# Kernel optimization log

Measured on AMD Instinct MI355X. Metric: run time of the kernel, lower is better.

The kernel has to match this reference:

```python
import jax, jax.numpy as jnp
import numpy as np

N, K, C, G = 100000, 16, 64, 8
EPS = 1e-5


def bn(x, gamma, beta):
    # training-mode BatchNorm1d over all dims except channel (last)
    axes = tuple(range(x.ndim - 1))
    m = jnp.mean(x, axis=axes)
    v = jnp.var(x, axis=axes)
    return (x - m) * jax.lax.rsqrt(v + EPS) * gamma + beta


def setup_inputs() -> dict:
    key = jax.random.key(0)
    ks = jax.random.split(key, 16)

    def lin(k, i, o):
        return (jax.random.normal(k, (i, o), jnp.float32) / np.sqrt(i)).astype(jnp.float32)

    feat = jax.random.normal(ks[0], (N, C), jnp.float32)
    coord = jax.random.uniform(ks[1], (N, 3), jnp.float32) * 10.0
    ref = jax.random.randint(ks[2], (N, K), 0, N)
    drop = jax.random.uniform(ks[3], (N, K)) < 0.05  # some padded (-1) neighbors
    ref = jnp.where(drop, -1, ref)

    return {
        "feat": feat, "coord": coord, "reference_index": ref,
        "wq": lin(ks[4], C, C), "bq": jnp.zeros((C,), jnp.float32),
        "gq": jnp.ones((C,), jnp.float32), "betaq": jnp.zeros((C,), jnp.float32),
        "wk": lin(ks[5], C, C), "bk": jnp.zeros((C,), jnp.float32),
        "gk": jnp.ones((C,), jnp.float32), "betak": jnp.zeros((C,), jnp.float32),
        "wv": lin(ks[6], C, C), "bv": jnp.zeros((C,), jnp.float32),
        "wp1": lin(ks[7], 3, C), "bp1": jnp.zeros((C,), jnp.float32),
        "gp": jnp.ones((C,), jnp.float32), "betap": jnp.zeros((C,), jnp.float32),
        "wp2": lin(ks[8], C, C), "bp2": jnp.zeros((C,), jnp.float32),
        "ww1": lin(ks[9], C, G), "bw1": jnp.zeros((G,), jnp.float32),
        "gw": jnp.ones((G,), jnp.float32), "betaw": jnp.zeros((G,), jnp.float32),
        "ww2": lin(ks[10], G, G), "bw2": jnp.zeros((G,), jnp.float32),
    }


def reference(feat, coord, reference_index,
              wq, bq, gq, betaq,
              wk, bk, gk, betak,
              wv, bv,
              wp1, bp1, gp, betap,
              wp2, bp2,
              ww1, bw1, gw, betaw,
              ww2, bw2):
    # q/k/v projections
    q = jax.nn.relu(bn(feat @ wq + bq, gq, betaq))   # [N, C]
    k = jax.nn.relu(bn(feat @ wk + bk, gk, betak))   # [N, C]
    v = feat @ wv + bv                                # [N, C]

    idx = jnp.clip(reference_index, 0, N - 1)         # clipped gather index [N, K]
    mask = (reference_index >= 0).astype(feat.dtype)  # sign(ref + 1)

    key_n = k[idx]                                    # [N, K, C] neighbor keys
    val = v[idx]                                      # [N, K, C]
    pos = coord[idx] - coord[:, None, :]              # [N, K, 3] relative coords

    relation_qk = key_n - q[:, None, :]               # [N, K, C]

    # pe_bias branch
    peb = jax.nn.relu(bn(pos @ wp1 + bp1, gp, betap)) @ wp2 + bp2  # [N, K, C]
    relation_qk = relation_qk + peb
    val = val + peb

    # weight encoding -> grouped softmax over neighbors, masked
    w = jax.nn.relu(bn(relation_qk @ ww1 + bw1, gw, betaw)) @ ww2 + bw2  # [N, K, G]
    w = jax.nn.softmax(w, axis=1) * mask[:, :, None]

    val = val.reshape(N, K, G, C // G)
    out = jnp.einsum('nsgi,nsg->ngi', val, w).reshape(N, C)
    return out
```

## Files before the change

### kernel.cpp

```cpp
#include <hip/hip_runtime.h>
#include <hip/hip_bf16.h>

#define NPTS 100000
#define KNBR 16
#define CCH  64
#define GRP  8
#define BN_EPS 1e-5f
#define NROW (NPTS * KNBR)
#define NBATCH (NROW / 64)
#define NPB   ((NPTS + 63) / 64)

#define O_QLINH 0
#define O_KLINH (NPTS * 32)
#define O_VLINH (NPTS * 64)
#define O_STAT  (NPTS * 96)
#define O_AFF   (O_STAT + 416)
#define O_W2W1  (O_AFF + 416)
#define O_BW1E  (O_W2W1 + 512)
#define O_QW1   (O_BW1E + 8)
#define O_KW1   (O_QW1 + NPTS * 8)
#define O_W1H   (O_KW1 + NPTS * 8)

typedef __attribute__((ext_vector_type(8))) short short8;
typedef __attribute__((ext_vector_type(4))) short short4v;
typedef __attribute__((ext_vector_type(4))) float f32x4;
#define MFMA16(a, b, c) __builtin_amdgcn_mfma_f32_16x16x32_bf16(a, b, c, 0, 0, 0)

__device__ __forceinline__ int clip_idx(int r) {
    int i = r < 0 ? 0 : r;
    return i >= NPTS ? NPTS - 1 : i;
}
__device__ __forceinline__ unsigned short f2bf(float x) {
    union { float f; unsigned u; } v; v.f = x;
    unsigned r = v.u + 0x7fffu + ((v.u >> 16) & 1u);
    return (unsigned short)(r >> 16);
}
__device__ __forceinline__ float bf2f(unsigned short h) {
    union { unsigned u; float f; } v; v.u = ((unsigned)h) << 16;
    return v.f;
}
__device__ __forceinline__ unsigned pk_bf16(float lo, float hi) {
    unsigned r;
    asm("v_cvt_pk_bf16_f32 %0, %1, %2" : "=v"(r) : "v"(lo), "v"(hi));
    return r;
}
__device__ __forceinline__ int physK(int s) {
    return (s >> 5) * 32 + ((s >> 2) & 3) * 8 + ((s >> 4) & 1) * 4 + (s & 3);
}
__device__ __forceinline__ int aOff(int r, int p) {
    return r * 64 + (((p >> 3) ^ (r & 7)) << 3) + (p & 7);
}
__device__ __forceinline__ int kib_of(int i, int q) {
    return (i < 4) ? (4 * q + i) : (16 + 4 * q + (i - 4));
}

__global__ __launch_bounds__(512) void k_prep(
    const float* __restrict__ wp2, const float* __restrict__ ww1,
    const float* __restrict__ bw1, const float* __restrict__ bp2,
    float* __restrict__ stat, float* __restrict__ w2w1, float* __restrict__ bw1e)
{
    int t = threadIdx.x;
    if (t < 416) stat[t] = 0.f;
    int j = t >> 3, g = t & 7;
    float acc = 0.f;
    #pragma unroll 16
    for (int c = 0; c < 64; ++c) acc = fmaf(wp2[j * 64 + c], ww1[c * 8 + g], acc);
    w2w1[t] = acc;
    if (t < 8) {
        float b = bw1[t];
        #pragma unroll 16
        for (int c = 0; c < 64; ++c) b = fmaf(bp2[c], ww1[c * 8 + t], b);
        bw1e[t] = b;
    }
}

#define QKV_BLOCKS 512
__global__ __launch_bounds__(256) void k_qkv(
    const float* __restrict__ feat,
    const float* __restrict__ wq, const float* __restrict__ bq,
    const float* __restrict__ wk, const float* __restrict__ bk,
    const float* __restrict__ wv, const float* __restrict__ bv,
    const float* __restrict__ bp2,
    const float* __restrict__ coord, const int* __restrict__ ref,
    short* __restrict__ QlinH, short* __restrict__ KlinH, short* __restrict__ VlinH,
    float* __restrict__ stat)
{
    __shared__ short sA[4096];
    __shared__ float s_red[9];
    const int tid = threadIdx.x, lane = tid & 63, w = tid >> 6;
    const int q = lane >> 4, c15 = lane & 15;

    if (blockIdx.x >= QKV_BLOCKS) {
        float m[9];
        #pragma unroll
        for (int i = 0; i < 9; ++i) m[i] = 0.f;
        const int gid = (blockIdx.x - QKV_BLOCKS) * 256 + tid;
        const int stride = 128 * 256;
        for (int row = gid; row < NROW; row += stride) {
            int n = row >> 4;
            int idx = clip_idx(ref[row]);
            float px = coord[idx * 3 + 0] - coord[n * 3 + 0];
            float py = coord[idx * 3 + 1] - coord[n * 3 + 1];
            float pz = coord[idx * 3 + 2] - coord[n * 3 + 2];
            m[0] += px; m[1] += py; m[2] += pz;
            m[3] = fmaf(px, px, m[3]); m[4] = fmaf(py, py, m[4]); m[5] = fmaf(pz, pz, m[5]);
            m[6] = fmaf(px, py, m[6]); m[7] = fmaf(px, pz, m[7]); m[8] = fmaf(py, pz, m[8]);
        }
        if (tid < 9) s_red[tid] = 0.f;
        __syncthreads();
        #pragma unroll
        for (int off = 32; off >= 1; off >>= 1) {
            #pragma unroll
            for (int i = 0; i < 9; ++i) m[i] += __shfl_xor(m[i], off, 64);
        }
        if (lane == 0) {
            #pragma unroll
            for (int i = 0; i < 9; ++i) atomicAdd(&s_red[i], m[i]);
        }
        __syncthreads();
        if (tid < 9) atomicAdd(&stat[256 + tid], s_red[tid]);
        return;
    }

    short8 bfrag[3][2];
    float bias[3];
    #pragma unroll
    for (int t = 0; t < 3; ++t) {
        int gt = w * 3 + t;
        const float* W = (gt < 4) ? wq : (gt < 8) ? wk : wv;
        const float* B = (gt < 4) ? bq : (gt < 8) ? bk : bv;
        int col = (gt * 16 + c15) & 63;
        bias[t] = B[col] + (gt >= 8 ? bp2[col] : 0.f);
        #pragma unroll
        for (int kt = 0; kt < 2; ++kt) {
            short8 bb;
            #pragma unroll
            for (int i = 0; i < 8; ++i) {
                int kk = kt * 32 + kib_of(i, q);
                bb[i] = (short)f2bf(W[kk * 64 + col]);
            }
            bfrag[t][kt] = bb;
        }
    }
    float st_s[3], st_q[3];
    #pragma unroll
    for (int t = 0; t < 3; ++t) { st_s[t] = 0.f; st_q[t] = 0.f; }

    const int c4 = c15 * 4;
    const int pk4 = physK(c4);

    for (int b = blockIdx.x; b < NPB; b += QKV_BLOCKS) {
        const int pbase = b * 64;
        #pragma unroll
        for (int i = 0; i < 4; ++i) {
            int p = w * 16 + i * 4 + q;
            int n = pbase + p;
            float4 v = make_float4(0.f, 0.f, 0.f, 0.f);
            if (n < NPTS) v = *(const float4*)(feat + n * 64 + c4);
            short4v h;
            h[0] = (short)f2bf(v.x); h[1] = (short)f2bf(v.y);
            h[2] = (short)f2bf(v.z); h[3] = (short)f2bf(v.w);
            *(short4v*)(sA + aOff(p, pk4)) = h;
        }
        __syncthreads();
        #pragma unroll
        for (int mt = 0; mt < 4; ++mt) {
            int r = mt * 16 + c15;
            int ch0 = q ^ (r & 7);
            int ch1 = (4 + q) ^ (r & 7);
            short8 a0 = *(const short8*)(sA + r * 64 + (ch0 << 3));
            short8 a1 = *(const short8*)(sA + r * 64 + (ch1 << 3));
            #pragma unroll
            for (int t = 0; t < 3; ++t) {
                f32x4 acc = (f32x4){0.f, 0.f, 0.f, 0.f};
                acc = MFMA16(a0, bfrag[t][0], acc);
                acc = MFMA16(a1, bfrag[t][1], acc);
                int gt = w * 3 + t;
                #pragma unroll
                for (int rg = 0; rg < 4; ++rg) {
                    int row = mt * 16 + 4 * q + rg;
                    int n = pbase + row;
                    if (n < NPTS) {
                        unsigned short h = f2bf(acc[rg] + bias[t]);
                        float vr = bf2f(h);
                        if (gt < 4)      QlinH[n * 64 + gt * 16 + c15] = (short)h;
                        else if (gt < 8) KlinH[n * 64 + (gt - 4) * 16 + c15] = (short)h;
                        else             VlinH[n * 64 + (gt - 8) * 16 + c15] = (short)h;
                        if (gt < 8) { st_s[t] += vr; st_q[t] = fmaf(vr, vr, st_q[t]); }
                    }
                }
            }
        }
        __syncthreads();
    }
    #pragma unroll
    for (int t = 0; t < 3; ++t) {
        st_s[t] += __shfl_xor(st_s[t], 16, 64); st_s[t] += __shfl_xor(st_s[t], 32, 64);
        st_q[t] += __shfl_xor(st_q[t], 16, 64); st_q[t] += __shfl_xor(st_q[t], 32, 64);
    }
    if (q == 0) {
        #pragma unroll
        for (int t = 0; t < 3; ++t) {
            int gt = w * 3 + t;
            if (gt < 4) {
                atomicAdd(&stat[gt * 16 + c15], st_s[t]);
                atomicAdd(&stat[64 + gt * 16 + c15], st_q[t]);
            } else if (gt < 8) {
                atomicAdd(&stat[128 + (gt - 4) * 16 + c15], st_s[t]);
                atomicAdd(&stat[192 + (gt - 4) * 16 + c15], st_q[t]);
            }
        }
    }
}

__global__ __launch_bounds__(192) void k_finA(
    const float* __restrict__ gq, const float* __restrict__ betaq,
    const float* __restrict__ gk, const float* __restrict__ betak,
    const float* __restrict__ gp, const float* __restrict__ betap,
    const float* __restrict__ wp1, const float* __restrict__ bp1,
    const float* __restrict__ stat, float* __restrict__ aff)
{
    int t = threadIdx.x;
    if (t < 64) {
        float m = stat[t] / (float)NPTS;
        float v = stat[64 + t] / (float)NPTS - m * m;
        float a = gq[t] * rsqrtf(v + BN_EPS);
        aff[t] = a;
        aff[64 + t] = betaq[t] - m * a;
    } else if (t < 128) {
        int c = t - 64;
        float m = stat[128 + c] / (float)NPTS;
        float v = stat[192 + c] / (float)NPTS - m * m;
        float a = gk[c] * rsqrtf(v + BN_EPS);
        aff[128 + c] = a;
        aff[192 + c] = betak[c] - m * a;
    } else {
        int c = t - 128;
        const float R = (float)NROW;
        float Ex = stat[256] / R, Ey = stat[257] / R, Ez = stat[258] / R;
        float Exx = stat[259] / R, Eyy = stat[260] / R, Ezz = stat[261] / R;
        float Exy = stat[262] / R, Exz = stat[263] / R, Eyz = stat[264] / R;
        float Cxx = Exx - Ex * Ex, Cyy = Eyy - Ey * Ey, Czz = Ezz - Ez * Ez;
        float Cxy = Exy - Ex * Ey, Cxz = Exz - Ex * Ez, Cyz = Eyz - Ey * Ez;
        float a0 = wp1[c], a1 = wp1[64 + c], a2 = wp1[128 + c];
        float mean = a0 * Ex + a1 * Ey + a2 * Ez + bp1[c];
        float var = a0 * a0 * Cxx + a1 * a1 * Cyy + a2 * a2 * Czz
                  + 2.f * (a0 * a1 * Cxy + a0 * a2 * Cxz + a1 * a2 * Cyz);
        float a = gp[c] * rsqrtf(var + BN_EPS);
        aff[256 + c] = a;
        aff[320 + c] = betap[c] - mean * a;
    }
}

__global__ __launch_bounds__(128) void k_qkw(
    const short* __restrict__ QlinH, const short* __restrict__ KlinH,
    const float* __restrict__ ww1, const float* __restrict__ aff,
    float* __restrict__ QW1, float* __restrict__ KW1)
{
    __shared__ short sA[2][8192];
    const int tid = threadIdx.x, lane = tid & 63, w = tid >> 6;
    const int q = lane >> 4, g = lane & 15;
    short8 bimg[2];
    #pragma unroll
    for (int kt = 0; kt < 2; ++kt) {
        short8 bb;
        #pragma unroll
        for (int i = 0; i < 8; ++i) {
            int s = kt * 32 + kib_of(i, q);
            bb[i] = (short)f2bf(g < 8 ? ww1[s * 8 + g] : 0.f);
        }
        bimg[kt] = bb;
    }
    const int r8 = lane >> 3, c8 = (lane & 7) * 8;
    f32x4 qa0 = *(const f32x4*)(aff + c8),       qa1 = *(const f32x4*)(aff + c8 + 4);
    f32x4 qb0 = *(const f32x4*)(aff + 64 + c8),  qb1 = *(const f32x4*)(aff + 64 + c8 + 4);
    f32x4 ka0 = *(const f32x4*)(aff + 128 + c8), ka1 = *(const f32x4*)(aff + 128 + c8 + 4);
    f32x4 kb0 = *(const f32x4*)(aff + 192 + c8), kb1 = *(const f32x4*)(aff + 192 + c8 + 4);
    const int pkA = physK(c8), pkB = physK(c8 + 4);
    short* AQ = sA[w];
    short* AK = sA[w] + 4096;

    for (int b = blockIdx.x * 2 + w; b < NPB; b += gridDim.x * 2) {
        const int pbase = b * 64;
        #pragma unroll
        for (int it = 0; it < 8; ++it) {
            int p = it * 8 + r8;
            int n = pbase + p;
            short8 qraw = {0,0,0,0,0,0,0,0}, kraw = {0,0,0,0,0,0,0,0};
            if (n < NPTS) {
                qraw = *(const short8*)(QlinH + n * 64 + c8);
                kraw = *(const short8*)(KlinH + n * 64 + c8);
            }
            float qf[8], kf[8];
            #pragma unroll
            for (int e = 0; e < 4; ++e) {
                qf[e]     = fmaxf(fmaf(bf2f((unsigned short)qraw[e]), qa0[e], qb0[e]), 0.f);
                qf[e + 4] = fmaxf(fmaf(bf2f((unsigned short)qraw[e + 4]), qa1[e], qb1[e]), 0.f);
                kf[e]     = fmaxf(fmaf(bf2f((unsigned short)kraw[e]), ka0[e], kb0[e]), 0.f);
                kf[e + 4] = fmaxf(fmaf(bf2f((unsigned short)kraw[e + 4]), ka1[e], kb1[e]), 0.f);
            }
            uint2 qv0 = make_uint2(pk_bf16(qf[0], qf[1]), pk_bf16(qf[2], qf[3]));
            uint2 qv1 = make_uint2(pk_bf16(qf[4], qf[5]), pk_bf16(qf[6], qf[7]));
            uint2 kv0 = make_uint2(pk_bf16(kf[0], kf[1]), pk_bf16(kf[2], kf[3]));
            uint2 kv1 = make_uint2(pk_bf16(kf[4], kf[5]), pk_bf16(kf[6], kf[7]));
            *(uint2*)(AQ + aOff(p, pkA)) = qv0;
            *(uint2*)(AQ + aOff(p, pkB)) = qv1;
            *(uint2*)(AK + aOff(p, pkA)) = kv0;
            *(uint2*)(AK + aOff(p, pkB)) = kv1;
        }
        #pragma unroll
        for (int mt = 0; mt < 4; ++mt) {
            f32x4 aq = (f32x4){0.f, 0.f, 0.f, 0.f};
            f32x4 ak = (f32x4){0.f, 0.f, 0.f, 0.f};
            int r = mt * 16 + g;
            #pragma unroll
            for (int kt = 0; kt < 2; ++kt) {
                int chunk = (kt * 4 + q) ^ (r & 7);
                aq = MFMA16(*(const short8*)(AQ + r * 64 + (chunk << 3)), bimg[kt], aq);
                ak = MFMA16(*(const short8*)(AK + r * 64 + (chunk << 3)), bimg[kt], ak);
            }
            if (g < 8) {
                #pragma unroll
                for (int rg = 0; rg < 4; ++rg) {
                    int n = pbase + mt * 16 + 4 * q + rg;
                    if (n < NPTS) {
                        QW1[n * 8 + g] = aq[rg];
                        KW1[n * 8 + g] = ak[rg];
                    }
                }
            }
        }
    }
}

__global__ __launch_bounds__(128) void k_wstats(
    const float* __restrict__ coord, const int* __restrict__ ref,
    const float* __restrict__ wp1, const float* __restrict__ bp1,
    const float* __restrict__ bw1e, const float* __restrict__ w2w1,
    const float* __restrict__ QW1, const float* __restrict__ KW1,
    const float* __restrict__ aff, float* __restrict__ stat,
    short* __restrict__ W1H)
{
    __shared__ short sP[2][4096];
    __shared__ float sPos[2][256];
    __shared__ int   sIdx[2][64];
    __shared__ float sRed[16];
    const int tid = threadIdx.x, lane = tid & 63, w = tid >> 6;
    const int q = lane >> 4, g = lane & 15, g7 = lane & 7;
    short8 bimg[2];
    #pragma unroll
    for (int kt = 0; kt < 2; ++kt) {
        short8 bb;
        #pragma unroll
        for (int i = 0; i < 8; ++i) {
            int s = kt * 32 + kib_of(i, q);
            bb[i] = (short)f2bf(g < 8 ? w2w1[s * 8 + g] : 0.f);
        }
        bimg[kt] = bb;
    }
    if (tid < 16) sRed[tid] = 0.f;
    __syncthreads();

    const int c2 = (lane & 31) * 2, rh5 = (lane >> 5) * 32;
    const float paL = aff[256 + c2],     paH = aff[256 + c2 + 1];
    const float A0L = paL * wp1[c2],       A0H = paH * wp1[c2 + 1];
    const float A1L = paL * wp1[64 + c2],  A1H = paH * wp1[64 + c2 + 1];
    const float A2L = paL * wp1[128 + c2], A2H = paH * wp1[128 + c2 + 1];
    const float B0L = fmaf(paL, bp1[c2], aff[320 + c2]);
    const float B0H = fmaf(paH, bp1[c2 + 1], aff[320 + c2 + 1]);
    const int pOff = physK(c2);
    const float bwg = bw1e[g7];

    short* P = sP[w];
    float* pos = sPos[w];
    int* idxs = sIdx[w];
    float accS = 0.f, accQ = 0.f;

    for (int b = blockIdx.x * 2 + w; b < NBATCH; b += gridDim.x * 2) {
        const int rbase = b * 64;
        const int p0 = b * 4;
        {
            int r = ref[rbase + lane];
            int idx = clip_idx(r);
            idxs[lane] = idx;
            int n = p0 + (lane >> 4);
            pos[lane * 4 + 0] = coord[idx * 3 + 0] - coord[n * 3 + 0];
            pos[lane * 4 + 1] = coord[idx * 3 + 1] - coord[n * 3 + 1];
            pos[lane * 4 + 2] = coord[idx * 3 + 2] - coord[n * 3 + 2];
        }
        float kwc[16], qwc[4];
        #pragma unroll
        for (int mt = 0; mt < 4; ++mt) {
            int4 i4 = *(const int4*)(idxs + mt * 16 + 4 * q);
            kwc[mt * 4 + 0] = KW1[i4.x * 8 + g7];
            kwc[mt * 4 + 1] = KW1[i4.y * 8 + g7];
            kwc[mt * 4 + 2] = KW1[i4.z * 8 + g7];
            kwc[mt * 4 + 3] = KW1[i4.w * 8 + g7];
            qwc[mt] = QW1[(p0 + mt) * 8 + g7];
        }
        #pragma unroll 8
        for (int rr = 0; rr < 32; ++rr) {
            int row = rh5 + rr;
            f32x4 pp = *(const f32x4*)(pos + row * 4);
            float lo = fmaxf(fmaf(pp.x, A0L, fmaf(pp.y, A1L, fmaf(pp.z, A2L, B0L))), 0.f);
            float hi = fmaxf(fmaf(pp.x, A0H, fmaf(pp.y, A1H, fmaf(pp.z, A2H, B0H))), 0.f);
            *(unsigned*)(P + aOff(row, pOff)) = pk_bf16(lo, hi);
        }
        #pragma unroll
        for (int mt = 0; mt < 4; ++mt) {
            f32x4 acc = (f32x4){0.f, 0.f, 0.f, 0.f};
            int r = mt * 16 + g;
            #pragma unroll
            for (int kt = 0; kt < 2; ++kt) {
                int chunk = (kt * 4 + q) ^ (r & 7);
                acc = MFMA16(*(const short8*)(P + r * 64 + (chunk << 3)), bimg[kt], acc);
            }
            if (g < 8) {
                float dq = bwg - qwc[mt];
                #pragma unroll
                for (int rg = 0; rg < 4; ++rg) {
                    float Wf = acc[rg] + kwc[mt * 4 + rg] + dq;
                    unsigned short wh = f2bf(Wf);
                    float Wr = bf2f(wh);
                    accS += Wr;
                    accQ = fmaf(Wr, Wr, accQ);
                    W1H[(rbase + mt * 16 + 4 * q + rg) * 8 + g7] = (short)wh;
                }
            }
        }
    }
    accS += __shfl_xor(accS, 16, 64); accS += __shfl_xor(accS, 32, 64);
    accQ += __shfl_xor(accQ, 16, 64); accQ += __shfl_xor(accQ, 32, 64);
    if (lane < 8) {
        atomicAdd(&sRed[lane], accS);
        atomicAdd(&sRed[8 + lane], accQ);
    }
    __syncthreads();
    if (tid < 16) atomicAdd(&stat[384 + tid], sRed[tid]);
}

__global__ __launch_bounds__(64) void k_finB(
    const float* __restrict__ gw_, const float* __restrict__ betaw,
    const float* __restrict__ stat, float* __restrict__ aff)
{
    int t = threadIdx.x;
    if (t < 8) {
        const float M = (float)NROW;
        float m = stat[384 + t] / M;
        float v = stat[392 + t] / M - m * m;
        float a = gw_[t] * rsqrtf(v + BN_EPS);
        aff[384 + t] = a;
        aff[392 + t] = betaw[t] - m * a;
    }
}

__global__ __launch_bounds__(128) void k_final(
    const float* __restrict__ coord, const int* __restrict__ ref,
    const float* __restrict__ wp1, const float* __restrict__ bp1,
    const float* __restrict__ wp2,
    const float* __restrict__ ww2, const float* __restrict__ bw2,
    const short* __restrict__ W1H, const short* __restrict__ VlinH,
    const float* __restrict__ aff, float* __restrict__ out)
{
    __shared__ short sP[2][4096];
    __shared__ float sPos[2][256];
    __shared__ int   sIdx[2][64];
    __shared__ float sWn[2][576];
    __shared__ float sW2[72];
    const int tid = threadIdx.x, lane = tid & 63, w = tid >> 6;
    const int q = lane >> 4, g15 = lane & 15;

    if (tid < 64) sW2[tid] = ww2[tid];
    else if (tid < 72) sW2[tid] = bw2[tid - 64];
    __syncthreads();

    short8 b1[8];
    #pragma unroll
    for (int tt = 0; tt < 8; ++tt) {
        int kt = tt & 1, nt = tt >> 1;
        short8 bb;
        #pragma unroll
        for (int i = 0; i < 8; ++i) {
            int kk = kt * 32 + kib_of(i, q);
            bb[i] = (short)f2bf(wp2[kk * 64 + nt * 16 + g15]);
        }
        b1[tt] = bb;
    }

    const int c2 = (lane & 31) * 2, rh5 = (lane >> 5) * 32;
    const float paL = aff[256 + c2],     paH = aff[256 + c2 + 1];
    const float A0L = paL * wp1[c2],       A0H = paH * wp1[c2 + 1];
    const float A1L = paL * wp1[64 + c2],  A1H = paH * wp1[64 + c2 + 1];
    const float A2L = paL * wp1[128 + c2], A2H = paH * wp1[128 + c2 + 1];
    const float B0L = fmaf(paL, bp1[c2], aff[320 + c2]);
    const float B0H = fmaf(paH, bp1[c2 + 1], aff[320 + c2 + 1]);
    const int pOff = physK(c2);
    float wa8[8], wb8[8];
    #pragma unroll
    for (int gg = 0; gg < 8; ++gg) {
        wa8[gg] = aff[384 + gg];
        wb8[gg] = aff[392 + gg];
    }

    short* P = sP[w];
    float* pos = sPos[w];
    int* idxs = sIdx[w];
    float* wn = sWn[w];

#define LOADV(MT, VC) do {                                              \
        int4 i4_ = *(const int4*)(idxs + (MT) * 16 + 4 * q);            \
        int ia_[4] = {i4_.x, i4_.y, i4_.z, i4_.w};                      \
        _Pragma("unroll")                                               \
        for (int rg = 0; rg < 4; ++rg) {                                \
            const short* vb_ = VlinH + ia_[rg] * 64 + g15;              \
            _Pragma("unroll")                                           \
            for (int nt = 0; nt < 4; ++nt)                              \
                VC[rg * 4 + nt] = (unsigned short)vb_[nt * 16];         \
        }                                                               \
    } while (0)

#define EINSUM_MT(MT, VC) do {                                          \
        int r_ = (MT) * 16 + g15;                                       \
        int c0_ = q ^ (r_ & 7);                                         \
        int c1_ = (4 + q) ^ (r_ & 7);                                   \
        short8 a0_ = *(const short8*)(P + r_ * 64 + (c0_ << 3));        \
        short8 a1_ = *(const short8*)(P + r_ * 64 + (c1_ << 3));        \
        const int ro0_ = ((MT) * 16 + 4 * q) * 9;                       \
        _Pragma("unroll")                                               \
        for (int nt = 0; nt < 4; ++nt) {                                \
            f32x4 acc_ = (f32x4){0.f, 0.f, 0.f, 0.f};                   \
            acc_ = MFMA16(a0_, b1[nt * 2 + 0], acc_);                   \
            acc_ = MFMA16(a1_, b1[nt * 2 + 1], acc_);                   \
            int col_ = nt * 16 + g15;                                   \
            int o_ = nt * 2 + (g15 >> 3);                               \
            float part_ = 0.f;                                          \
            _Pragma("unroll")                                           \
            for (int rg = 0; rg < 4; ++rg) {                            \
                float v_ = bf2f(VC[rg * 4 + nt]);                       \
                part_ = fmaf(v_ + acc_[rg], wn[ro0_ + rg * 9 + o_], part_); \
            }                                                           \
            part_ += __shfl_xor(part_, 16, 64);                         \
            part_ += __shfl_xor(part_, 32, 64);                         \
            if (q == 0) out[(p0 + (MT)) * 64 + col_] = part_;           \
        }                                                               \
    } while (0)

    for (int b = blockIdx.x * 2 + w; b < NBATCH; b += gridDim.x * 2) {
        const int rbase = b * 64;
        const int p0 = b * 4;
        {
            int r = ref[rbase + lane];
            int idx = clip_idx(r);
            idxs[lane] = idx;
            int n = p0 + (lane >> 4);
            pos[lane * 4 + 0] = coord[idx * 3 + 0] - coord[n * 3 + 0];
            pos[lane * 4 + 1] = coord[idx * 3 + 1] - coord[n * 3 + 1];
            pos[lane * 4 + 2] = coord[idx * 3 + 2] - coord[n * 3 + 2];
            pos[lane * 4 + 3] = (r >= 0) ? 1.f : 0.f;
        }
        short8 w8 = *(const short8*)(W1H + (rbase + lane) * 8);
        unsigned short vcA[16], vcB[16], vcC[16], vcD[16];
        LOADV(0, vcA);
        LOADV(1, vcB);
        #pragma unroll 8
        for (int rr = 0; rr < 32; ++rr) {
            int row = rh5 + rr;
            f32x4 pp = *(const f32x4*)(pos + row * 4);
            float lo = fmaxf(fmaf(pp.x, A0L, fmaf(pp.y, A1L, fmaf(pp.z, A2L, B0L))), 0.f);
            float hi = fmaxf(fmaf(pp.x, A0H, fmaf(pp.y, A1H, fmaf(pp.z, A2H, B0H))), 0.f);
            *(unsigned*)(P + aOff(row, pOff)) = pk_bf16(lo, hi);
        }
        LOADV(2, vcC);
        LOADV(3, vcD);
        {
            float h[8];
            #pragma unroll
            for (int gg = 0; gg < 8; ++gg) {
                float Wf = bf2f((unsigned short)w8[gg]);
                h[gg] = fmaxf(fmaf(wa8[gg], Wf, wb8[gg]), 0.f);
            }
            float mask = pos[lane * 4 + 3];
            #pragma unroll
            for (int o = 0; o < 8; ++o) {
                float acc = sW2[64 + o];
                #pragma unroll
                for (int gg = 0; gg < 8; ++gg) acc = fmaf(h[gg], sW2[gg * 8 + o], acc);
                float e = __expf(acc);
                float s = e;
                s += __shfl_xor(s, 1, 64);
                s += __shfl_xor(s, 2, 64);
                s += __shfl_xor(s, 4, 64);
                s += __shfl_xor(s, 8, 64);
                wn[lane * 9 + o] = e * __builtin_amdgcn_rcpf(s) * mask;
            }
        }
        EINSUM_MT(0, vcA);
        EINSUM_MT(1, vcB);
        EINSUM_MT(2, vcC);
        EINSUM_MT(3, vcD);
    }
#undef LOADV
#undef EINSUM_MT
}

extern "C" void kernel_launch(void* const* d_in, const int* in_sizes, int n_in,
                              void* d_out, int out_size, void* d_ws, size_t ws_size,
                              hipStream_t stream)
{
    const float* feat  = (const float*)d_in[0];
    const float* coord = (const float*)d_in[1];
    const int*   ref   = (const int*)d_in[2];
    const float* wq    = (const float*)d_in[3];
    const float* bq    = (const float*)d_in[4];
    const float* gq    = (const float*)d_in[5];
    const float* betaq = (const float*)d_in[6];
    const float* wk    = (const float*)d_in[7];
    const float* bk    = (const float*)d_in[8];
    const float* gk    = (const float*)d_in[9];
    const float* betak = (const float*)d_in[10];
    const float* wv    = (const float*)d_in[11];
    const float* bv    = (const float*)d_in[12];
    const float* wp1   = (const float*)d_in[13];
    const float* bp1   = (const float*)d_in[14];
    const float* gp    = (const float*)d_in[15];
    const float* betap = (const float*)d_in[16];
    const float* wp2   = (const float*)d_in[17];
    const float* bp2   = (const float*)d_in[18];
    const float* ww1   = (const float*)d_in[19];
    const float* bw1   = (const float*)d_in[20];
    const float* gw_   = (const float*)d_in[21];
    const float* betaw = (const float*)d_in[22];
    const float* ww2   = (const float*)d_in[23];
    const float* bw2   = (const float*)d_in[24];

    float* ws    = (float*)d_ws;
    short* QlinH = (short*)(ws + O_QLINH);
    short* KlinH = (short*)(ws + O_KLINH);
    short* VlinH = (short*)(ws + O_VLINH);
    float* stat  = ws + O_STAT;
    float* aff   = ws + O_AFF;
    float* w2w1  = ws + O_W2W1;
    float* bw1e  = ws + O_BW1E;
    float* QW1   = ws + O_QW1;
    float* KW1   = ws + O_KW1;
    short* W1H   = (short*)(ws + O_W1H);
    float* out   = (float*)d_out;

    hipLaunchKernelGGL(k_prep, dim3(1), dim3(512), 0, stream,
                       wp2, ww1, bw1, bp2, stat, w2w1, bw1e);
    hipLaunchKernelGGL(k_qkv, dim3(QKV_BLOCKS + 128), dim3(256), 0, stream,
                       feat, wq, bq, wk, bk, wv, bv, bp2, coord, ref,
                       QlinH, KlinH, VlinH, stat);
    hipLaunchKernelGGL(k_finA, dim3(1), dim3(192), 0, stream,
                       gq, betaq, gk, betak, gp, betap, wp1, bp1, stat, aff);
    hipLaunchKernelGGL(k_qkw, dim3(782), dim3(128), 0, stream,
                       QlinH, KlinH, ww1, aff, QW1, KW1);
    hipLaunchKernelGGL(k_wstats, dim3(2500), dim3(128), 0, stream,
                       coord, ref, wp1, bp1, bw1e, w2w1, QW1, KW1, aff, stat, W1H);
    hipLaunchKernelGGL(k_finB, dim3(1), dim3(64), 0, stream, gw_, betaw, stat, aff);
    hipLaunchKernelGGL(k_final, dim3(2500), dim3(128), 0, stream,
                       coord, ref, wp1, bp1, wp2, ww2, bw2,
                       W1H, VlinH, aff, out);
}
```

Baseline: 215.4 us.

## Fold finB into final kernel, stage V gathers via LDS with coalesced rows

Drops the k_finB launch, so each k_final block now computes the weight-BN affine itself from the stats. k_final becomes one wave per block (6250 blocks), and the neighbour V rows are gathered with short8-wide coalesced loads into a padded LDS tile instead of scattered per-lane short loads held in registers. k_qkv is remapped so each wave handles one column group for Q, K and V, which removes per-tile branching and cuts atomics. The cost is more LDS traffic, an extra LDS pass over V, and redundant BN-finalize work in every block.

```diff
diff --git a/kernel.cpp b/kernel.cpp
--- a/kernel.cpp
+++ b/kernel.cpp
@@ -122,29 +122,29 @@
         return;
     }
 
+    const int colg = w * 16 + c15;
     short8 bfrag[3][2];
     float bias[3];
-    #pragma unroll
-    for (int t = 0; t < 3; ++t) {
-        int gt = w * 3 + t;
-        const float* W = (gt < 4) ? wq : (gt < 8) ? wk : wv;
-        const float* B = (gt < 4) ? bq : (gt < 8) ? bk : bv;
-        int col = (gt * 16 + c15) & 63;
-        bias[t] = B[col] + (gt >= 8 ? bp2[col] : 0.f);
-        #pragma unroll
-        for (int kt = 0; kt < 2; ++kt) {
-            short8 bb;
-            #pragma unroll
-            for (int i = 0; i < 8; ++i) {
-                int kk = kt * 32 + kib_of(i, q);
-                bb[i] = (short)f2bf(W[kk * 64 + col]);
-            }
-            bfrag[t][kt] = bb;
-        }
-    }
-    float st_s[3], st_q[3];
-    #pragma unroll
-    for (int t = 0; t < 3; ++t) { st_s[t] = 0.f; st_q[t] = 0.f; }
+    {
+        const float* Ws[3] = {wq, wk, wv};
+        bias[0] = bq[colg];
+        bias[1] = bk[colg];
+        bias[2] = bv[colg] + bp2[colg];
+        #pragma unroll
+        for (int t = 0; t < 3; ++t) {
+            #pragma unroll
+            for (int kt = 0; kt < 2; ++kt) {
+                short8 bb;
+                #pragma unroll
+                for (int i = 0; i < 8; ++i) {
+                    int kk = kt * 32 + kib_of(i, q);
+                    bb[i] = (short)f2bf(Ws[t][kk * 64 + colg]);
+                }
+                bfrag[t][kt] = bb;
+            }
+        }
+    }
+    float qs = 0.f, qs2 = 0.f, ks = 0.f, ks2 = 0.f;
 
     const int c4 = c15 * 4;
     const int pk4 = physK(c4);
@@ -175,41 +175,38 @@
                 f32x4 acc = (f32x4){0.f, 0.f, 0.f, 0.f};
                 acc = MFMA16(a0, bfrag[t][0], acc);
                 acc = MFMA16(a1, bfrag[t][1], acc);
-                int gt = w * 3 + t;
                 #pragma unroll
                 for (int rg = 0; rg < 4; ++rg) {
                     int row = mt * 16 + 4 * q + rg;
                     int n = pbase + row;
                     if (n < NPTS) {
                         unsigned short h = f2bf(acc[rg] + bias[t]);
-                        float vr = bf2f(h);
-                        if (gt < 4)      QlinH[n * 64 + gt * 16 + c15] = (short)h;
-                        else if (gt < 8) KlinH[n * 64 + (gt - 4) * 16 + c15] = (short)h;
-                        else             VlinH[n * 64 + (gt - 8) * 16 + c15] = (short)h;
-                        if (gt < 8) { st_s[t] += vr; st_q[t] = fmaf(vr, vr, st_q[t]); }
+                        if (t == 0) {
+                            QlinH[n * 64 + colg] = (short)h;
+                            float vr = bf2f(h);
+                            qs += vr; qs2 = fmaf(vr, vr, qs2);
+                        } else if (t == 1) {
+                            KlinH[n * 64 + colg] = (short)h;
+                            float vr = bf2f(h);
+                            ks += vr; ks2 = fmaf(vr, vr, ks2);
+                        } else {
+                            VlinH[n * 64 + colg] = (short)h;
+                        }
                     }
                 }
             }
         }
         __syncthreads();
     }
-    #pragma unroll
-    for (int t = 0; t < 3; ++t) {
-        st_s[t] += __shfl_xor(st_s[t], 16, 64); st_s[t] += __shfl_xor(st_s[t], 32, 64);
-        st_q[t] += __shfl_xor(st_q[t], 16, 64); st_q[t] += __shfl_xor(st_q[t], 32, 64);
-    }
+    qs += __shfl_xor(qs, 16, 64);  qs += __shfl_xor(qs, 32, 64);
+    qs2 += __shfl_xor(qs2, 16, 64); qs2 += __shfl_xor(qs2, 32, 64);
+    ks += __shfl_xor(ks, 16, 64);  ks += __shfl_xor(ks, 32, 64);
+    ks2 += __shfl_xor(ks2, 16, 64); ks2 += __shfl_xor(ks2, 32, 64);
     if (q == 0) {
-        #pragma unroll
-        for (int t = 0; t < 3; ++t) {
-            int gt = w * 3 + t;
-            if (gt < 4) {
-                atomicAdd(&stat[gt * 16 + c15], st_s[t]);
-                atomicAdd(&stat[64 + gt * 16 + c15], st_q[t]);
-            } else if (gt < 8) {
-                atomicAdd(&stat[128 + (gt - 4) * 16 + c15], st_s[t]);
-                atomicAdd(&stat[192 + (gt - 4) * 16 + c15], st_q[t]);
-            }
-        }
+        atomicAdd(&stat[colg], qs);
+        atomicAdd(&stat[64 + colg], qs2);
+        atomicAdd(&stat[128 + colg], ks);
+        atomicAdd(&stat[192 + colg], ks2);
     }
 }
 
@@ -439,39 +436,27 @@
     if (tid < 16) atomicAdd(&stat[384 + tid], sRed[tid]);
 }
 
-__global__ __launch_bounds__(64) void k_finB(
-    const float* __restrict__ gw_, const float* __restrict__ betaw,
-    const float* __restrict__ stat, float* __restrict__ aff)
-{
-    int t = threadIdx.x;
-    if (t < 8) {
-        const float M = (float)NROW;
-        float m = stat[384 + t] / M;
-        float v = stat[392 + t] / M - m * m;
-        float a = gw_[t] * rsqrtf(v + BN_EPS);
-        aff[384 + t] = a;
-        aff[392 + t] = betaw[t] - m * a;
-    }
-}
-
-__global__ __launch_bounds__(128) void k_final(
+__global__ __launch_bounds__(64) void k_final(
     const float* __restrict__ coord, const int* __restrict__ ref,
     const float* __restrict__ wp1, const float* __restrict__ bp1,
     const float* __restrict__ wp2,
     const float* __restrict__ ww2, const float* __restrict__ bw2,
+    const float* __restrict__ gw_, const float* __restrict__ betaw,
     const short* __restrict__ W1H, const short* __restrict__ VlinH,
-    const float* __restrict__ aff, float* __restrict__ out)
+    const float* __restrict__ aff, const float* __restrict__ stat,
+    float* __restrict__ out)
 {
-    __shared__ short sP[2][4096];
-    __shared__ float sPos[2][256];
-    __shared__ int   sIdx[2][64];
-    __shared__ float sWn[2][576];
+    __shared__ short sP[4096];
+    __shared__ short sV[64 * 72];
+    __shared__ float sPos[256];
+    __shared__ int   sIdx[64];
+    __shared__ float sWn[576];
     __shared__ float sW2[72];
-    const int tid = threadIdx.x, lane = tid & 63, w = tid >> 6;
+    const int lane = threadIdx.x;
     const int q = lane >> 4, g15 = lane & 15;
 
-    if (tid < 64) sW2[tid] = ww2[tid];
-    else if (tid < 72) sW2[tid] = bw2[tid - 64];
+    sW2[lane] = ww2[lane];
+    if (lane < 8) sW2[64 + lane] = bw2[lane];
     __syncthreads();
 
     short8 b1[8];
@@ -498,34 +483,23 @@
     float wa8[8], wb8[8];
     #pragma unroll
     for (int gg = 0; gg < 8; ++gg) {
-        wa8[gg] = aff[384 + gg];
-        wb8[gg] = aff[392 + gg];
-    }
-
-    short* P = sP[w];
-    float* pos = sPos[w];
-    int* idxs = sIdx[w];
-    float* wn = sWn[w];
-
-#define LOADV(MT, VC) do {                                              \
-        int4 i4_ = *(const int4*)(idxs + (MT) * 16 + 4 * q);            \
-        int ia_[4] = {i4_.x, i4_.y, i4_.z, i4_.w};                      \
-        _Pragma("unroll")                                               \
-        for (int rg = 0; rg < 4; ++rg) {                                \
-            const short* vb_ = VlinH + ia_[rg] * 64 + g15;              \
-            _Pragma("unroll")                                           \
-            for (int nt = 0; nt < 4; ++nt)                              \
-                VC[rg * 4 + nt] = (unsigned short)vb_[nt * 16];         \
-        }                                                               \
-    } while (0)
-
-#define EINSUM_MT(MT, VC) do {                                          \
+        const float M = (float)NROW;
+        float m = stat[384 + gg] / M;
+        float v = stat[392 + gg] / M - m * m;
+        float a = gw_[gg] * rsqrtf(v + BN_EPS);
+        wa8[gg] = a;
+        wb8[gg] = betaw[gg] - m * a;
+    }
+    const int vr8 = lane >> 3, vc8 = (lane & 7) * 8;
+
+#define EINSUM_MT(MT) do {                                              \
         int r_ = (MT) * 16 + g15;                                       \
         int c0_ = q ^ (r_ & 7);                                         \
         int c1_ = (4 + q) ^ (r_ & 7);                                   \
-        short8 a0_ = *(const short8*)(P + r_ * 64 + (c0_ << 3));        \
-        short8 a1_ = *(const short8*)(P + r_ * 64 + (c1_ << 3));        \
-        const int ro0_ = ((MT) * 16 + 4 * q) * 9;                       \
+        short8 a0_ = *(const short8*)(sP + r_ * 64 + (c0_ << 3));       \
+        short8 a1_ = *(const short8*)(sP + r_ * 64 + (c1_ << 3));       \
+        const int vrow0_ = (MT) * 16 + 4 * q;                           \
+        const int ro0_ = vrow0_ * 9;                                    \
         _Pragma("unroll")                                               \
         for (int nt = 0; nt < 4; ++nt) {                                \
             f32x4 acc_ = (f32x4){0.f, 0.f, 0.f, 0.f};                   \
@@ -536,8 +510,8 @@
             float part_ = 0.f;                                          \
             _Pragma("unroll")                                           \
             for (int rg = 0; rg < 4; ++rg) {                            \
-                float v_ = bf2f(VC[rg * 4 + nt]);                       \
-                part_ = fmaf(v_ + acc_[rg], wn[ro0_ + rg * 9 + o_], part_); \
+                float v_ = bf2f((unsigned short)sV[(vrow0_ + rg) * 72 + col_]); \
+                part_ = fmaf(v_ + acc_[rg], sWn[ro0_ + rg * 9 + o_], part_); \
             }                                                           \
             part_ += __shfl_xor(part_, 16, 64);                         \
             part_ += __shfl_xor(part_, 32, 64);                         \
@@ -545,33 +519,35 @@
         }                                                               \
     } while (0)
 
-    for (int b = blockIdx.x * 2 + w; b < NBATCH; b += gridDim.x * 2) {
+    for (int b = blockIdx.x; b < NBATCH; b += gridDim.x) {
         const int rbase = b * 64;
         const int p0 = b * 4;
         {
             int r = ref[rbase + lane];
             int idx = clip_idx(r);
-            idxs[lane] = idx;
+            sIdx[lane] = idx;
             int n = p0 + (lane >> 4);
-            pos[lane * 4 + 0] = coord[idx * 3 + 0] - coord[n * 3 + 0];
-            pos[lane * 4 + 1] = coord[idx * 3 + 1] - coord[n * 3 + 1];
-            pos[lane * 4 + 2] = coord[idx * 3 + 2] - coord[n * 3 + 2];
-            pos[lane * 4 + 3] = (r >= 0) ? 1.f : 0.f;
+            sPos[lane * 4 + 0] = coord[idx * 3 + 0] - coord[n * 3 + 0];
+            sPos[lane * 4 + 1] = coord[idx * 3 + 1] - coord[n * 3 + 1];
+            sPos[lane * 4 + 2] = coord[idx * 3 + 2] - coord[n * 3 + 2];
+            sPos[lane * 4 + 3] = (r >= 0) ? 1.f : 0.f;
         }
         short8 w8 = *(const short8*)(W1H + (rbase + lane) * 8);
-        unsigned short vcA[16], vcB[16], vcC[16], vcD[16];
-        LOADV(0, vcA);
-        LOADV(1, vcB);
+        #pragma unroll
+        for (int it = 0; it < 8; ++it) {
+            int row = it * 8 + vr8;
+            int idx = sIdx[row];
+            *(short8*)(sV + row * 72 + vc8) =
+                *(const short8*)(VlinH + idx * 64 + vc8);
+        }
         #pragma unroll 8
         for (int rr = 0; rr < 32; ++rr) {
             int row = rh5 + rr;
-            f32x4 pp = *(const f32x4*)(pos + row * 4);
+            f32x4 pp = *(const f32x4*)(sPos + row * 4);
             float lo = fmaxf(fmaf(pp.x, A0L, fmaf(pp.y, A1L, fmaf(pp.z, A2L, B0L))), 0.f);
             float hi = fmaxf(fmaf(pp.x, A0H, fmaf(pp.y, A1H, fmaf(pp.z, A2H, B0H))), 0.f);
-            *(unsigned*)(P + aOff(row, pOff)) = pk_bf16(lo, hi);
-        }
-        LOADV(2, vcC);
-        LOADV(3, vcD);
+            *(unsigned*)(sP + aOff(row, pOff)) = pk_bf16(lo, hi);
+        }
         {
             float h[8];
             #pragma unroll
@@ -579,7 +555,7 @@
                 float Wf = bf2f((unsigned short)w8[gg]);
                 h[gg] = fmaxf(fmaf(wa8[gg], Wf, wb8[gg]), 0.f);
             }
-            float mask = pos[lane * 4 + 3];
+            float mask = sPos[lane * 4 + 3];
             #pragma unroll
             for (int o = 0; o < 8; ++o) {
                 float acc = sW2[64 + o];
@@ -591,15 +567,14 @@
                 s += __shfl_xor(s, 2, 64);
                 s += __shfl_xor(s, 4, 64);
                 s += __shfl_xor(s, 8, 64);
-                wn[lane * 9 + o] = e * __builtin_amdgcn_rcpf(s) * mask;
-            }
-        }
-        EINSUM_MT(0, vcA);
-        EINSUM_MT(1, vcB);
-        EINSUM_MT(2, vcC);
-        EINSUM_MT(3, vcD);
-    }
-#undef LOADV
+                sWn[lane * 9 + o] = e * __builtin_amdgcn_rcpf(s) * mask;
+            }
+        }
+        EINSUM_MT(0);
+        EINSUM_MT(1);
+        EINSUM_MT(2);
+        EINSUM_MT(3);
+    }
 #undef EINSUM_MT
 }
 
@@ -657,8 +632,7 @@
                        QlinH, KlinH, ww1, aff, QW1, KW1);
     hipLaunchKernelGGL(k_wstats, dim3(2500), dim3(128), 0, stream,
                        coord, ref, wp1, bp1, bw1e, w2w1, QW1, KW1, aff, stat, W1H);
-    hipLaunchKernelGGL(k_finB, dim3(1), dim3(64), 0, stream, gw_, betaw, stat, aff);
-    hipLaunchKernelGGL(k_final, dim3(2500), dim3(128), 0, stream,
-                       coord, ref, wp1, bp1, wp2, ww2, bw2,
-                       W1H, VlinH, aff, out);
-}
+    hipLaunchKernelGGL(k_final, dim3(6250), dim3(64), 0, stream,
+                       coord, ref, wp1, bp1, wp2, ww2, bw2, gw_, betaw,
+                       W1H, VlinH, aff, stat, out);
+}
```

New measurement: 220.1 us. 1.02x slower.
